# Optimization experiments

Hardware: AMD Instinct MI355X
Metric: run time of the kernel (lower is better)

The kernel has to match this reference:

```python
import jax, jax.numpy as jnp
import numpy as np

N = 100000   # nodes
E = 1600000  # edges (avg degree 16)
F_IN, H1, H2, H3, C = 500, 200, 100, 40, 3


def setup_inputs() -> dict:
    key = jax.random.key(0)
    ks = jax.random.split(key, 10)
    def w(k, shape, fan_in):
        return jax.random.normal(k, shape, dtype=jnp.float32) / np.sqrt(fan_in)
    return {
        "x": jax.random.normal(ks[0], (N, F_IN), dtype=jnp.float32),
        "edge_index": jax.random.randint(ks[1], (2, E), 0, N, dtype=jnp.int32),
        "W1": w(ks[2], (H1, F_IN), F_IN), "b1": jnp.zeros((H1,), jnp.float32),
        "W1b": w(ks[3], (H2, H1), H1),  "b1b": jnp.zeros((H2,), jnp.float32),
        "W2b": w(ks[4], (H3, H2), H2),  "b2b": jnp.zeros((H3,), jnp.float32),
        "W2": w(ks[5], (C, H3), H3),    "b2": jnp.zeros((C,), jnp.float32),
    }


def _gcn_conv(x, W, b, src, dst, norm_e, n):
    # GCNConv: linear transform, then normalized scatter-add aggregation, then bias
    h = x @ W.T                                   # [N, out]
    msgs = h[src] * norm_e[:, None]               # [E+N, out] gathered, normalized
    out = jax.ops.segment_sum(msgs, dst, num_segments=n)
    return out + b


def reference(x, edge_index, W1, b1, W1b, b1b, W2b, b2b, W2, b2):
    n = x.shape[0]
    loop = jnp.arange(n, dtype=edge_index.dtype)
    src = jnp.concatenate([edge_index[0], loop])  # add self-loops (GCNConv default)
    dst = jnp.concatenate([edge_index[1], loop])
    # symmetric normalization: deg computed on target nodes, norm = d^-1/2[src]*d^-1/2[dst]
    deg = jax.ops.segment_sum(jnp.ones_like(dst, dtype=x.dtype), dst, num_segments=n)
    dinv = jnp.where(deg > 0, jax.lax.rsqrt(deg), 0.0)
    norm_e = dinv[src] * dinv[dst]

    # dropout(p=0.5, training=self.training) is identity at inference
    h = jax.nn.relu(_gcn_conv(x, W1, b1, src, dst, norm_e, n))
    h = jax.nn.relu(_gcn_conv(h, W1b, b1b, src, dst, norm_e, n))
    h = jax.nn.relu(_gcn_conv(h, W2b, b2b, src, dst, norm_e, n))
    return _gcn_conv(h, W2, b2, src, dst, norm_e, n)
```

## Files before the change

### kernel.cpp

```cpp
#include <hip/hip_runtime.h>


#define DEV __device__ __forceinline__

typedef __attribute__((ext_vector_type(8))) short short8;
typedef __attribute__((ext_vector_type(8))) _Float16 f16x8;
typedef __attribute__((ext_vector_type(4))) float f32x4;
typedef __attribute__((ext_vector_type(4))) _Float16 f16x4;

DEV void gload_lds16(const void* g, void* l) {
    __builtin_amdgcn_global_load_lds(
        (const __attribute__((address_space(1))) unsigned int*)g,
        (__attribute__((address_space(3))) unsigned int*)l, 16, 0, 0);
}


__global__ void k_init(int* __restrict__ cnt, int* __restrict__ fill, int n) {
    int i = blockIdx.x * 256 + threadIdx.x;
    if (i < n) { cnt[i] = 1; fill[i] = 0; }
}

__global__ void k_count(const int* __restrict__ dst, int* __restrict__ cnt, int E) {
    int e = blockIdx.x * 256 + threadIdx.x;
    if (e < E) atomicAdd(&cnt[dst[e]], 1);
}

__global__ void k_scan1(const int* __restrict__ cnt, int* __restrict__ row_start,
                        int* __restrict__ partial, float* __restrict__ dinv, int n) {
    __shared__ int sdata[256];
    int base = blockIdx.x * 1024;
    int t = threadIdx.x;
    int v[4]; int sum = 0;
#pragma unroll
    for (int j = 0; j < 4; ++j) {
        int idx = base + t * 4 + j;
        v[j] = (idx < n) ? cnt[idx] : 0;
        if (idx < n) dinv[idx] = rsqrtf((float)v[j]);
        sum += v[j];
    }
    sdata[t] = sum;
    __syncthreads();
    for (int off = 1; off < 256; off <<= 1) {
        int x = (t >= off) ? sdata[t - off] : 0;
        __syncthreads();
        sdata[t] += x;
        __syncthreads();
    }
    int excl = sdata[t] - sum;
#pragma unroll
    for (int j = 0; j < 4; ++j) {
        int idx = base + t * 4 + j;
        if (idx < n) row_start[idx] = excl;
        excl += v[j];
    }
    if (t == 255) partial[blockIdx.x] = sdata[255];
}

__global__ void k_scan2(int* __restrict__ partial, int nb) {
    __shared__ int s[128];
    int t = threadIdx.x;
    int v = (t < nb) ? partial[t] : 0;
    s[t] = v;
    __syncthreads();
    for (int off = 1; off < 128; off <<= 1) {
        int x = (t >= off) ? s[t - off] : 0;
        __syncthreads();
        s[t] += x;
        __syncthreads();
    }
    if (t < nb) partial[t] = s[t] - v;
}

__global__ void k_scan3(int* __restrict__ row_start, const int* __restrict__ partial,
                        int n, int total) {
    int i = blockIdx.x * 256 + threadIdx.x;
    if (i < n) row_start[i] += partial[i >> 10];
    if (i == 0) row_start[n] = total;
}

__global__ void k_fill(const int* __restrict__ src, const int* __restrict__ dst,
                       const int* __restrict__ row_start, int* __restrict__ fill,
                       int* __restrict__ csr_src, int E, int n) {
    int i = blockIdx.x * 256 + threadIdx.x;
    int total = E + n;
    if (i >= total) return;
    int s, d;
    if (i < E) { s = src[i]; d = dst[i]; }
    else       { s = d = i - E; }
    int pos = row_start[d] + atomicAdd(&fill[d], 1);
    csr_src[pos] = s;
}


__global__ void k_wcvt16(const float* __restrict__ W, int N, int K,
                         unsigned short* __restrict__ Wh, int NPAD, int KPAD) {
    int i = blockIdx.x * 256 + threadIdx.x;
    if (i >= NPAD * KPAD) return;
    int r = i / KPAD, k = i - r * KPAD;
    float x = (r < N && k < K) ? W[r * K + k] : 0.f;
    Wh[i] = __builtin_bit_cast(unsigned short, (_Float16)x);
}

__global__ void k_wdec16(const float* __restrict__ W, int N, int K,
                         unsigned short* __restrict__ Wh, unsigned short* __restrict__ Wl,
                         int NPAD, int KPAD) {
    int i = blockIdx.x * 256 + threadIdx.x;
    if (i >= NPAD * KPAD) return;
    int r = i / KPAD, k = i - r * KPAD;
    float x = (r < N && k < K) ? W[r * K + k] : 0.f;
    _Float16 h = (_Float16)x;
    _Float16 l = (_Float16)((x - (float)h) * 2048.0f);
    Wh[i] = __builtin_bit_cast(unsigned short, h);
    Wl[i] = __builtin_bit_cast(unsigned short, l);
}


struct A8 { f32x4 lo, hi; };

template <int NFC, int KPH, int NPH, int HILO, int MODE, typename AT>
__global__ __launch_bounds__(512, 4)
void gemm_res(const AT* __restrict__ A, int lda, int M, int K,
              const unsigned short* __restrict__ Wh,
              const unsigned short* __restrict__ Wl,
              const float* __restrict__ dinv,
              _Float16* __restrict__ H16, int ldh, int Nout) {
    constexpr int NPAD = NFC * 16;
    constexpr int KP   = KPH * NPH;
    constexpr int CHH  = NPAD * KPH / 8;
    constexpr int CHT  = CHH * (1 + HILO);
    constexpr int NIT  = (CHT + 511) / 512;
    constexpr int SB   = NPAD * 64;
    constexpr int HB   = CHH * 16;
    constexpr int SPP  = KPH / 32;
    constexpr int NS   = SPP * NPH;
    constexpr int D    = 2;
    __shared__ char lds[CHT * 16];

    const int tid  = threadIdx.x;
    const int wv   = tid >> 6;
    const int lane = tid & 63;
    const int lr   = lane & 15;
    const int kq   = lane >> 4;
    const int m0   = blockIdx.y * 128;
    const int col0 = blockIdx.x * NPAD;

    const unsigned short* WhB = Wh + (size_t)col0 * KP;
    const unsigned short* WlB = Wl + (size_t)col0 * KP;

    auto stageW = [&](int p) {
#pragma unroll
        for (int i = 0; i < NIT; ++i) {
            int c = tid + i * 512;
            if ((CHT % 512 == 0) || (c < CHT)) {
                int h  = (HILO && c >= CHH) ? 1 : 0;
                int cc = c - h * CHH;
                int st = cc / (NPAD * 4);
                int rm = cc - st * (NPAD * 4);
                int r  = rm >> 2;
                int sl = rm & 3;
                int gs = sl ^ (r & 3);
                const unsigned short* gp = (h ? WlB : WhB)
                    + (size_t)r * KP + p * KPH + st * 32 + gs * 8;
                gload_lds16(gp, lds + (size_t)c * 16);
            }
        }
    };

    int arow = m0 + wv * 16 + lr;
    if (arow >= M) arow = M - 1;
    const AT* Arow = A + (size_t)arow * lda;

    auto loadA32 = [&](int s) -> A8 {
        A8 o;
        int kb = s * 32 + kq * 8;
        if (kb + 8 <= K) {
            const float* ap = (const float*)Arow + kb;
            o.lo = *(const f32x4*)ap;
            o.hi = *(const f32x4*)(ap + 4);
        } else {
#pragma unroll
            for (int i = 0; i < 4; ++i) {
                int k0 = kb + i, k1 = kb + 4 + i;
                o.lo[i] = (k0 < K) ? (float)Arow[k0] : 0.f;
                o.hi[i] = (k1 < K) ? (float)Arow[k1] : 0.f;
            }
        }
        return o;
    };
    auto loadA16 = [&](int s) -> short8 {
        int kb = s * 32 + kq * 8;
        if (kb + 8 <= K) return *(const short8*)((const unsigned short*)Arow + kb);
        short8 o;
        const unsigned short* ap = (const unsigned short*)Arow;
#pragma unroll
        for (int i = 0; i < 8; ++i) o[i] = (kb + i < K) ? (short)ap[kb + i] : (short)0;
        return o;
    };
    auto cvtA = [&](const A8& a) -> f16x8 {
        f16x8 o;
#pragma unroll
        for (int i = 0; i < 4; ++i) {
            o[i]     = (_Float16)a.lo[i];
            o[4 + i] = (_Float16)a.hi[i];
        }
        return o;
    };

    stageW(0);
    A8 ab[D]; short8 hb[D];
#pragma unroll
    for (int p = 0; p < D; ++p) {
        if (p < NS) {
            if constexpr (MODE == 0) ab[p] = loadA32(p);
            else                     hb[p] = loadA16(p);
        }
    }

    f32x4 ac[NFC], al[NFC];
#pragma unroll
    for (int f = 0; f < NFC; ++f) {
        ac[f] = (f32x4){0.f, 0.f, 0.f, 0.f};
        al[f] = (f32x4){0.f, 0.f, 0.f, 0.f};
    }

    __syncthreads();

    const int ro = lr * 64 + ((kq ^ (lr & 3)) << 4);

#pragma unroll
    for (int p = 0; p < NPH; ++p) {
#pragma unroll
        for (int sl = 0; sl < SPP; ++sl) {
            const int s = p * SPP + sl;
            f16x8 a0;
            if constexpr (MODE == 0) a0 = cvtA(ab[s % D]);
            else                     a0 = __builtin_bit_cast(f16x8, hb[s % D]);

            if (s + D < NS) {
                if constexpr (MODE == 0) ab[s % D] = loadA32(s + D);
                else                     hb[s % D] = loadA16(s + D);
            }

            const char* bb = lds + sl * SB;
#pragma unroll
            for (int f = 0; f < NFC; ++f) {
                f16x8 bh = __builtin_bit_cast(f16x8, *(const short8*)(bb + f * 1024 + ro));
                ac[f] = __builtin_amdgcn_mfma_f32_16x16x32_f16(a0, bh, ac[f], 0, 0, 0);
                if constexpr (HILO) {
                    f16x8 bl = __builtin_bit_cast(f16x8, *(const short8*)(bb + HB + f * 1024 + ro));
                    al[f] = __builtin_amdgcn_mfma_f32_16x16x32_f16(a0, bl, al[f], 0, 0, 0);
                }
            }
        }
        if (p + 1 < NPH) {
            __syncthreads();
            stageW(p + 1);
            __syncthreads();
        }
    }

    const int rbase = m0 + wv * 16 + kq * 4;
    float dv[4];
#pragma unroll
    for (int j = 0; j < 4; ++j) {
        int row = rbase + j;
        dv[j] = (row < M) ? dinv[row] : 0.f;
    }
#pragma unroll
    for (int f = 0; f < NFC; ++f) {
        int col = col0 + f * 16 + lr;
        if (col >= Nout) continue;
#pragma unroll
        for (int j = 0; j < 4; ++j) {
            int row = rbase + j;
            if (row >= M) continue;
            float v = ac[f][j];
            if constexpr (HILO) v += al[f][j] * (1.0f / 2048.0f);
            H16[(size_t)row * ldh + col] = (_Float16)(v * dv[j]);
        }
    }
}


template <int F, int VEC, bool RELU>
__global__ __launch_bounds__(256)
void agg_f16(const _Float16* __restrict__ h, const int* __restrict__ row_start,
             const int* __restrict__ csr_src, const float* __restrict__ dinv,
             const float* __restrict__ bias, _Float16* __restrict__ out, int n,
             int ldo) {
    constexpr int LPN = F / VEC;
    constexpr int NPW = 64 / LPN;
    int wave = blockIdx.x * 4 + (threadIdx.x >> 6);
    int lane = threadIdx.x & 63;
    int sub  = lane / LPN;
    int fi   = lane - sub * LPN;
    int node = wave * NPW + sub;
    if (sub >= NPW || node >= n) return;
    int f = fi * VEC;
    const _Float16* hf = h + f;

    f32x4 acc0 = {0.f, 0.f, 0.f, 0.f};
    f32x4 acc1 = {0.f, 0.f, 0.f, 0.f};

    auto addv = [&](const _Float16* p) {
        if constexpr (VEC == 8) {
            f16x8 v = *(const f16x8*)p;
            f16x4 vl, vh;
#pragma unroll
            for (int j = 0; j < 4; ++j) { vl[j] = v[j]; vh[j] = v[4 + j]; }
            acc0 += __builtin_convertvector(vl, f32x4);
            acc1 += __builtin_convertvector(vh, f32x4);
        } else {
            f16x4 v = *(const f16x4*)p;
            acc0 += __builtin_convertvector(v, f32x4);
        }
    };

    int e0 = row_start[node], e1 = row_start[node + 1];
    int e = e0;
    for (; e + 4 <= e1; e += 4) {
        int s0 = csr_src[e + 0];
        int s1 = csr_src[e + 1];
        int s2 = csr_src[e + 2];
        int s3 = csr_src[e + 3];
        const _Float16* p0 = &hf[(size_t)s0 * F];
        const _Float16* p1 = &hf[(size_t)s1 * F];
        const _Float16* p2 = &hf[(size_t)s2 * F];
        const _Float16* p3 = &hf[(size_t)s3 * F];
        addv(p0); addv(p1); addv(p2); addv(p3);
    }
    for (; e < e1; ++e) addv(&hf[(size_t)csr_src[e] * F]);

    float dn = dinv[node];
    if constexpr (VEC == 8) {
        f32x4 b0 = *(const f32x4*)&bias[f];
        f32x4 b1 = *(const f32x4*)&bias[f + 4];
        acc0 = acc0 * dn + b0;
        acc1 = acc1 * dn + b1;
        if (RELU) {
#pragma unroll
            for (int j = 0; j < 4; ++j) { acc0[j] = fmaxf(acc0[j], 0.f); acc1[j] = fmaxf(acc1[j], 0.f); }
        }
        f16x8 o;
#pragma unroll
        for (int j = 0; j < 4; ++j) { o[j] = (_Float16)acc0[j]; o[4 + j] = (_Float16)acc1[j]; }
        *(f16x8*)&out[(size_t)node * ldo + f] = o;
    } else {
        f32x4 b4 = *(const f32x4*)&bias[f];
        acc0 = acc0 * dn + b4;
        if (RELU) {
#pragma unroll
            for (int j = 0; j < 4; ++j) acc0[j] = fmaxf(acc0[j], 0.f);
        }
        f16x4 o;
#pragma unroll
        for (int j = 0; j < 4; ++j) o[j] = (_Float16)acc0[j];
        *(f16x4*)&out[(size_t)node * ldo + f] = o;
    }
}


__global__ void gemm_small(const _Float16* __restrict__ A, const float* __restrict__ B,
                           const float* __restrict__ dinv, float* __restrict__ C,
                           int M, int K) {
    int m = blockIdx.x * 256 + threadIdx.x;
    if (m >= M) return;
    float a0 = 0.f, a1 = 0.f, a2 = 0.f;
    for (int k = 0; k < K; ++k) {
        float a = (float)A[(size_t)m * K + k];
        a0 += a * B[0 * K + k];
        a1 += a * B[1 * K + k];
        a2 += a * B[2 * K + k];
    }
    float dv = dinv[m];
    C[(size_t)m * 3 + 0] = a0 * dv;
    C[(size_t)m * 3 + 1] = a1 * dv;
    C[(size_t)m * 3 + 2] = a2 * dv;
}

__global__ void agg_f3(const float* __restrict__ h, const int* __restrict__ row_start,
                       const int* __restrict__ csr_src, const float* __restrict__ dinv,
                       const float* __restrict__ bias, float* __restrict__ out, int n) {
    int i = blockIdx.x * 256 + threadIdx.x;
    if (i >= n * 3) return;
    int node = i / 3;
    int f = i - node * 3;
    float acc = 0.f;
    int e1 = row_start[node + 1];
    for (int e = row_start[node]; e < e1; ++e) {
        int s = csr_src[e];
        acc += h[(size_t)s * 3 + f];
    }
    out[i] = acc * dinv[node] + bias[f];
}


extern "C" void kernel_launch(void* const* d_in, const int* in_sizes, int n_in,
                              void* d_out, int out_size, void* d_ws, size_t ws_size,
                              hipStream_t stream) {
    const float* x   = (const float*)d_in[0];
    const int*   ei  = (const int*)d_in[1];
    const float* W1  = (const float*)d_in[2];
    const float* b1  = (const float*)d_in[3];
    const float* W1b = (const float*)d_in[4];
    const float* b1b = (const float*)d_in[5];
    const float* W2b = (const float*)d_in[6];
    const float* b2b = (const float*)d_in[7];
    const float* W2  = (const float*)d_in[8];
    const float* b2  = (const float*)d_in[9];
    float* out = (float*)d_out;

    const int F_IN = 500, H1 = 200, H2 = 100, H3 = 40;
    const int N = in_sizes[0] / F_IN;
    const int E = in_sizes[1] / 2;
    const int* src = ei;
    const int* dst = ei + E;

    size_t off = 0;
    auto alloc = [&](size_t bytes) -> void* {
        void* p = (char*)d_ws + off;
        off += (bytes + 255) & ~(size_t)255;
        return p;
    };
    int*   cnt       = (int*)  alloc((size_t)N * 4);
    int*   row_start = (int*)  alloc((size_t)(N + 1) * 4);
    int*   fill      = (int*)  alloc((size_t)N * 4);
    int*   partial   = (int*)  alloc(128 * 4);
    float* dinv      = (float*)alloc((size_t)N * 4);
    int*   csr_src   = (int*)  alloc((size_t)(E + N) * 4);
    unsigned short* wh1 = (unsigned short*)alloc(224 * 512 * 2);
    unsigned short* wh2 = (unsigned short*)alloc(128 * 256 * 2);
    unsigned short* wl2 = (unsigned short*)alloc(128 * 256 * 2);
    unsigned short* wh3 = (unsigned short*)alloc( 64 * 128 * 2);
    unsigned short* wl3 = (unsigned short*)alloc( 64 * 128 * 2);
    _Float16* h16   = (_Float16*)alloc((size_t)N * H1 * 2);
    _Float16* act16 = (_Float16*)alloc((size_t)N * H1 * 2);
    float*    bufC  = (float*)   alloc((size_t)N * 3 * 4);

    int gN  = (N + 255) / 256;
    int gE  = (E + 255) / 256;
    int gEN = (E + N + 255) / 256;
    int nb  = (N + 1023) / 1024;

    k_init <<<gN, 256, 0, stream>>>(cnt, fill, N);
    k_count<<<gE, 256, 0, stream>>>(dst, cnt, E);
    k_scan1<<<nb, 256, 0, stream>>>(cnt, row_start, partial, dinv, N);
    k_scan2<<<1, 128, 0, stream>>>(partial, nb);
    k_scan3<<<gN, 256, 0, stream>>>(row_start, partial, N, E + N);
    k_fill <<<gEN, 256, 0, stream>>>(src, dst, row_start, fill, csr_src, E, N);

    k_wcvt16<<<(224 * 512 + 255) / 256, 256, 0, stream>>>(W1,  H1, F_IN, wh1, 224, 512);
    k_wdec16<<<(128 * 256 + 255) / 256, 256, 0, stream>>>(W1b, H2, H1, wh2, wl2, 128, 256);
    k_wdec16<<<( 64 * 128 + 255) / 256, 256, 0, stream>>>(W2b, H3, H2, wh3, wl3,  64, 128);

    const int gR = (N + 127) / 128;

    gemm_res<14, 128, 4, 0, 0, float><<<dim3(1, gR), 512, 0, stream>>>(
        x, F_IN, N, F_IN, wh1, wh1, dinv, h16, H1, H1);
    {
        int waves = (N + 1) / 2, blocks = (waves + 3) / 4;
        agg_f16<200, 8, true><<<blocks, 256, 0, stream>>>(h16, row_start, csr_src, dinv,
                                                          b1, act16, N, 200);
    }
    gemm_res<4, 128, 2, 1, 1, _Float16><<<dim3(2, gR), 512, 0, stream>>>(
        act16, 200, N, H1, wh2, wl2, dinv, h16, H2, H2);
    agg_f16<100, 4, true><<<(N / 2 + 3) / 4, 256, 0, stream>>>(h16, row_start, csr_src, dinv,
                                                               b1b, act16, N, 112);
    gemm_res<4, 128, 1, 1, 1, _Float16><<<dim3(1, gR), 512, 0, stream>>>(
        act16, 112, N, H2, wh3, wl3, dinv, h16, H3, H3);
    {
        int waves = (N + 11) / 12, blocks = (waves + 3) / 4;
        agg_f16<40, 8, true><<<blocks, 256, 0, stream>>>(h16, row_start, csr_src, dinv,
                                                         b2b, act16, N, 40);
    }
    gemm_small<<<(N + 255) / 256, 256, 0, stream>>>(act16, W2, dinv, bufC, N, H3);
    agg_f3<<<(N * 3 + 255) / 256, 256, 0, stream>>>(bufC, row_start, csr_src, dinv,
                                                    b2, out, N);
}
```

Before: 549.9 us.

## Record per-edge rank during counting to drop fill atomics; deepen GEMM pipeline

The count kernel now saves the atomicAdd return value as each edge's rank within its destination row. The fill kernel then computes the CSR position directly instead of doing a second atomic per edge, and self-loops go to the last slot of each row. This removes the fill array and one pass of contended atomics, but adds an E-sized rank array that must be written and read back. The GEMM pipeline depth constant D also goes from 2 to 3, which may change prefetch depth.

```diff
diff --git a/kernel.cpp b/kernel.cpp
--- a/kernel.cpp
+++ b/kernel.cpp
@@ -15,14 +15,15 @@
 }
 
 
-__global__ void k_init(int* __restrict__ cnt, int* __restrict__ fill, int n) {
-    int i = blockIdx.x * 256 + threadIdx.x;
-    if (i < n) { cnt[i] = 1; fill[i] = 0; }
-}
-
-__global__ void k_count(const int* __restrict__ dst, int* __restrict__ cnt, int E) {
+__global__ void k_init(int* __restrict__ cnt, int n) {
+    int i = blockIdx.x * 256 + threadIdx.x;
+    if (i < n) cnt[i] = 0;
+}
+
+__global__ void k_count(const int* __restrict__ dst, int* __restrict__ cnt,
+                        int* __restrict__ rank, int E) {
     int e = blockIdx.x * 256 + threadIdx.x;
-    if (e < E) atomicAdd(&cnt[dst[e]], 1);
+    if (e < E) rank[e] = atomicAdd(&cnt[dst[e]], 1);
 }
 
 __global__ void k_scan1(const int* __restrict__ cnt, int* __restrict__ row_start,
@@ -34,7 +35,7 @@
 #pragma unroll
     for (int j = 0; j < 4; ++j) {
         int idx = base + t * 4 + j;
-        v[j] = (idx < n) ? cnt[idx] : 0;
+        v[j] = (idx < n) ? (cnt[idx] + 1) : 0;
         if (idx < n) dinv[idx] = rsqrtf((float)v[j]);
         sum += v[j];
     }
@@ -79,15 +80,21 @@
 }
 
 __global__ void k_fill(const int* __restrict__ src, const int* __restrict__ dst,
-                       const int* __restrict__ row_start, int* __restrict__ fill,
-                       int* __restrict__ csr_src, int E, int n) {
+                       const int* __restrict__ row_start, const int* __restrict__ cnt,
+                       const int* __restrict__ rank, int* __restrict__ csr_src,
+                       int E, int n) {
     int i = blockIdx.x * 256 + threadIdx.x;
     int total = E + n;
     if (i >= total) return;
-    int s, d;
-    if (i < E) { s = src[i]; d = dst[i]; }
-    else       { s = d = i - E; }
-    int pos = row_start[d] + atomicAdd(&fill[d], 1);
+    int s, pos;
+    if (i < E) {
+        s = src[i];
+        int d = dst[i];
+        pos = row_start[d] + rank[i];
+    } else {
+        s = i - E;
+        pos = row_start[s] + cnt[s];
+    }
     csr_src[pos] = s;
 }
 
@@ -133,7 +140,7 @@
     constexpr int HB   = CHH * 16;
     constexpr int SPP  = KPH / 32;
     constexpr int NS   = SPP * NPH;
-    constexpr int D    = 2;
+    constexpr int D    = 3;
     __shared__ char lds[CHT * 16];
 
     const int tid  = threadIdx.x;
@@ -424,7 +431,7 @@
     };
     int*   cnt       = (int*)  alloc((size_t)N * 4);
     int*   row_start = (int*)  alloc((size_t)(N + 1) * 4);
-    int*   fill      = (int*)  alloc((size_t)N * 4);
+    int*   rank      = (int*)  alloc((size_t)E * 4);
     int*   partial   = (int*)  alloc(128 * 4);
     float* dinv      = (float*)alloc((size_t)N * 4);
     int*   csr_src   = (int*)  alloc((size_t)(E + N) * 4);
@@ -442,12 +449,12 @@
     int gEN = (E + N + 255) / 256;
     int nb  = (N + 1023) / 1024;
 
-    k_init <<<gN, 256, 0, stream>>>(cnt, fill, N);
-    k_count<<<gE, 256, 0, stream>>>(dst, cnt, E);
+    k_init <<<gN, 256, 0, stream>>>(cnt, N);
+    k_count<<<gE, 256, 0, stream>>>(dst, cnt, rank, E);
     k_scan1<<<nb, 256, 0, stream>>>(cnt, row_start, partial, dinv, N);
     k_scan2<<<1, 128, 0, stream>>>(partial, nb);
     k_scan3<<<gN, 256, 0, stream>>>(row_start, partial, N, E + N);
-    k_fill <<<gEN, 256, 0, stream>>>(src, dst, row_start, fill, csr_src, E, N);
+    k_fill <<<gEN, 256, 0, stream>>>(src, dst, row_start, cnt, rank, csr_src, E, N);
 
     k_wcvt16<<<(224 * 512 + 255) / 256, 256, 0, stream>>>(W1,  H1, F_IN, wh1, 224, 512);
     k_wdec16<<<(128 * 256 + 255) / 256, 256, 0, stream>>>(W1b, H2, H1, wh2, wl2, 128, 256);
```

Result: faster. 507.0 us (-7.8%).
